# Performance work log

Measured on AMD Instinct MI355X. Metric: run time of the kernel, lower is better.

The kernel has to match this reference:

```python
import jax, jax.numpy as jnp
import numpy as np

NUM_HEADS = 8


def setup_inputs() -> dict:
    key = jax.random.key(0)
    ks = jax.random.split(key, 7)
    b, t, prompt_dim, emb_dim = 2, 4096, 256, 512
    hidden = emb_dim  # head_dim=None -> hidden_dim = emb_dim
    def xavier(k, fan_in, fan_out):
        limit = np.sqrt(6.0 / (fan_in + fan_out)).astype(np.float32)
        return jax.random.uniform(k, (fan_in, fan_out), jnp.float32, -limit, limit)
    return {
        "prompt": jax.random.normal(ks[0], (b, t, prompt_dim), jnp.float32),
        "Wp": xavier(ks[1], prompt_dim, emb_dim),
        "bp": jnp.zeros((emb_dim,), jnp.float32),
        "Wqkv": xavier(ks[2], emb_dim, 3 * hidden),
        "bqkv": jnp.zeros((3 * hidden,), jnp.float32),
        "Wo": xavier(ks[3], hidden, prompt_dim),
        "bo": jnp.zeros((prompt_dim,), jnp.float32),
    }


def reference(prompt, Wp, bp, Wqkv, bqkv, Wo, bo):
    # prompt_proj
    x = prompt @ Wp + bp                      # [b, t, emb_dim]
    b, t, c = x.shape
    qkv = x @ Wqkv + bqkv                     # [b, t, 3*hidden]
    q, k, v = jnp.split(qkv, 3, axis=2)
    def to_heads(z):
        return z.reshape(b, t, NUM_HEADS, -1).transpose(0, 2, 1, 3)  # [b, h, t, d]
    q, k, v = to_heads(q), to_heads(k), to_heads(v)
    d = k.shape[-1]
    scores = jnp.einsum("bhid,bhjd->bhij", q, k) / jnp.sqrt(jnp.float32(d))
    attn = jax.nn.softmax(scores, axis=-1)    # dropout = identity (eval)
    out = jnp.einsum("bhij,bhjd->bhid", attn, v)
    out = out.transpose(0, 2, 1, 3).reshape(b, t, -1)  # [b, t, hidden]
    return out @ Wo + bo                      # [b, t, prompt_dim]
```

## Files before the change

### kernel.cpp

```cpp
#include <hip/hip_runtime.h>
#include <math.h>
#include <stdint.h>


typedef unsigned short u16;
typedef __attribute__((ext_vector_type(8))) __bf16 bf16x8;
typedef __attribute__((ext_vector_type(4))) __bf16 bf16x4;
typedef __attribute__((ext_vector_type(4))) float f32x4;

#define AS1 __attribute__((address_space(1)))
#define AS3 __attribute__((address_space(3)))

__device__ __forceinline__ void async16(const void* g, void* l) {
  __builtin_amdgcn_global_load_lds((const AS1 void*)g, (AS3 void*)l, 16, 0, 0);
}

__device__ __forceinline__ u16 f2bf(float f) {
  union { float f; unsigned u; } c; c.f = f;
  return (u16)((c.u + 0x7fffu + ((c.u >> 16) & 1u)) >> 16);
}

__global__ void prep_kernel(const float* __restrict__ prompt, u16* __restrict__ pbf,
                            const float* __restrict__ Wp, u16* __restrict__ wpB,
                            const float* __restrict__ Wqkv, u16* __restrict__ wqkvT,
                            const float* __restrict__ Wo, u16* __restrict__ woT,
                            const float* __restrict__ bp, const float* __restrict__ bqkv,
                            float* __restrict__ bfused) {
  __shared__ u16 T[64][72];
  const int bid = blockIdx.x, tid = threadIdx.x;
  if (bid < 2688) {
    int i = bid * 256 + tid;
    if (i < 524288) {
      float4 v = ((const float4*)prompt)[i];
      ushort4 o;
      o.x = f2bf(v.x); o.y = f2bf(v.y); o.z = f2bf(v.z); o.w = f2bf(v.w);
      ((ushort4*)pbf)[i] = o;
    } else if (i < 557056) {
      int j = i - 524288;
      float4 v = ((const float4*)Wp)[j];
      ushort4 o;
      o.x = f2bf(v.x); o.y = f2bf(v.y); o.z = f2bf(v.z); o.w = f2bf(v.w);
      ((ushort4*)wpB)[j] = o;
    } else {
      int j = i - 557056; int n = j >> 9, k = j & 511;
      woT[j] = f2bf(Wo[k * 256 + n]);
    }
  } else if (bid < 2712) {
    __shared__ float red[256];
    const int nloc = tid & 63, slice = tid >> 6;
    const int n = (bid - 2688) * 64 + nloc;
    float s = 0.f;
#pragma unroll 8
    for (int e = slice * 128; e < slice * 128 + 128; e++) s += bp[e] * Wqkv[e * 1536 + n];
    red[tid] = s;
    __syncthreads();
    if (slice == 0)
      bfused[n] = red[nloc] + red[64 + nloc] + red[128 + nloc] + red[192 + nloc] + bqkv[n];
  } else {
    const int b = bid - 2712;
    const int k0 = (b & 7) * 64, n0 = (b >> 3) * 64;
    const int kl = tid >> 2, c4 = (tid & 3) * 16;
#pragma unroll
    for (int u = 0; u < 4; u++) {
      float4 v = *(const float4*)&Wqkv[(k0 + kl) * 1536 + n0 + c4 + 4 * u];
      T[kl][c4 + 4 * u + 0] = f2bf(v.x);
      T[kl][c4 + 4 * u + 1] = f2bf(v.y);
      T[kl][c4 + 4 * u + 2] = f2bf(v.z);
      T[kl][c4 + 4 * u + 3] = f2bf(v.w);
    }
    __syncthreads();
    const int nl = tid >> 2, kc = (tid & 3) * 16;
    u16 tmp[16];
#pragma unroll
    for (int e = 0; e < 16; e++) tmp[e] = T[kc + e][nl];
    *(uint4*)&wqkvT[(n0 + nl) * 512 + k0 + kc] = *(const uint4*)&tmp[0];
    *(uint4*)&wqkvT[(n0 + nl) * 512 + k0 + kc + 8] = *(const uint4*)&tmp[8];
  }
}

template <int TM, int TN, int MODE>
__global__ __launch_bounds__(256) void gemm_bt(
    const u16* __restrict__ A, const u16* __restrict__ Bt, const float* __restrict__ bias,
    float* __restrict__ outf, u16* __restrict__ outb,
    u16* __restrict__ qO, u16* __restrict__ kO, u16* __restrict__ vO,
    int M, int N, int K) {
  constexpr int MI = TM / 32, NJ = TN / 32;
  constexpr int NDMA = TM / 64 + TN / 64;
  __shared__ __align__(16) u16 As[2][TM * 32];
  __shared__ __align__(16) u16 Bs[2][TN * 32];
  const int tid = threadIdx.x;
  const int lane = tid & 63, w = tid >> 6;
  const int wr = w >> 1, wc = w & 1;
  const int lr = lane >> 4, lc = lane & 15;
  const long tileM = (long)blockIdx.y * TM;
  const long tileN = (long)blockIdx.x * TN;

  f32x4 acc[MI][NJ];
#pragma unroll
  for (int a = 0; a < MI; a++)
#pragma unroll
    for (int b = 0; b < NJ; b++) acc[a][b] = (f32x4){0.f, 0.f, 0.f, 0.f};

  const int r0 = lane >> 2;
  const int blk = lane & 3;

  auto stage = [&](int buf, int k0) {
#pragma unroll
    for (int i = 0; i < TM / 64; i++) {
      int r = w * (TM / 4) + i * 16 + r0;
      int g = (blk ^ ((r >> 1) & 3)) << 3;
      async16(A + (tileM + r) * (long)K + k0 + g, (void*)&As[buf][(w * (TM / 4) + i * 16) * 32]);
    }
#pragma unroll
    for (int i = 0; i < TN / 64; i++) {
      int r = w * (TN / 4) + i * 16 + r0;
      int g = (blk ^ ((r >> 1) & 3)) << 3;
      async16(Bt + (tileN + r) * (long)K + k0 + g, (void*)&Bs[buf][(w * (TN / 4) + i * 16) * 32]);
    }
  };

  stage(0, 0);
  for (int k0 = 0; k0 < K; k0 += 32) {
    const int cur = (k0 >> 5) & 1;
    stage(cur ^ 1, (k0 + 32 < K) ? k0 + 32 : 0);
    if constexpr (NDMA == 4) asm volatile("s_waitcnt vmcnt(4)" ::: "memory");
    else if constexpr (NDMA == 3) asm volatile("s_waitcnt vmcnt(3)" ::: "memory");
    else asm volatile("s_waitcnt vmcnt(2)" ::: "memory");
    asm volatile("s_barrier" ::: "memory");

    bf16x8 af[MI], bfv[NJ];
#pragma unroll
    for (int mi = 0; mi < MI; mi++) {
      int r = wr * (TM / 2) + mi * 16 + lc;
      af[mi] = *(const bf16x8*)&As[cur][r * 32 + ((lr ^ ((r >> 1) & 3)) << 3)];
    }
#pragma unroll
    for (int nj = 0; nj < NJ; nj++) {
      int r = wc * (TN / 2) + nj * 16 + lc;
      bfv[nj] = *(const bf16x8*)&Bs[cur][r * 32 + ((lr ^ ((r >> 1) & 3)) << 3)];
    }
#pragma unroll
    for (int mi = 0; mi < MI; mi++)
#pragma unroll
      for (int nj = 0; nj < NJ; nj++)
        acc[mi][nj] = __builtin_amdgcn_mfma_f32_16x16x32_bf16(af[mi], bfv[nj], acc[mi][nj], 0, 0, 0);
    asm volatile("s_barrier" ::: "memory");
  }

#pragma unroll
  for (int mi = 0; mi < MI; mi++)
#pragma unroll
    for (int nj = 0; nj < NJ; nj++) {
      long col = tileN + wc * (TN / 2) + nj * 16 + lc;
      long row0 = tileM + wr * (TM / 2) + mi * 16 + lr * 4;
      if constexpr (MODE == 1) {
        float bcol = bias[col];
        int sec = (int)(col >> 9);
        int c2 = (int)(col & 511);
        int h = c2 >> 6, d = c2 & 63;
        long pl = (row0 >> 12) * 8 + h;
        long t0 = row0 & 4095;
        if (sec == 2) {
          ushort4 pk;
          pk.x = f2bf(acc[mi][nj][0] + bcol);
          pk.y = f2bf(acc[mi][nj][1] + bcol);
          pk.z = f2bf(acc[mi][nj][2] + bcol);
          pk.w = f2bf(acc[mi][nj][3] + bcol);
          *(ushort4*)&vO[(pl * 64 + d) * 4096 + t0] = pk;
        } else {
          u16* dst = sec ? kO : qO;
          const float sc = sec ? 1.f : 0.18033688f;
#pragma unroll
          for (int r = 0; r < 4; r++)
            dst[((pl * 4096 + t0 + r) << 6) + d] = f2bf((acc[mi][nj][r] + bcol) * sc);
        }
      } else if constexpr (MODE == 2) {
        float bcol = bias[col];
#pragma unroll
        for (int r = 0; r < 4; r++)
          outf[(row0 + r) * (long)N + col] = acc[mi][nj][r] + bcol;
      } else {
#pragma unroll
        for (int r = 0; r < 4; r++)
          outb[(row0 + r) * (long)N + col] = f2bf(acc[mi][nj][r]);
      }
    }
}

__global__ __launch_bounds__(256) void flash_attn(
    const u16* __restrict__ Q, const u16* __restrict__ Kg,
    const u16* __restrict__ VTg, u16* __restrict__ Og) {
  __shared__ __align__(16) u16 KV[2][16384];
  __shared__ __align__(16) u16 Ps[4 * 2048];

  const int tid = threadIdx.x, lane = tid & 63, w = tid >> 6;
  const int lr = lane >> 4, lc = lane & 15;
  const int plane = blockIdx.y;
  const long pbase = (long)plane << 18;
  const int qr0 = blockIdx.x * 128 + w * 32;

  bf16x8 bq[2][2];
#pragma unroll
  for (int qi = 0; qi < 2; qi++)
#pragma unroll
    for (int kk = 0; kk < 2; kk++)
      bq[qi][kk] = *(const bf16x8*)&Q[pbase + (long)(qr0 + qi * 16 + lc) * 64 + kk * 32 + lr * 8];

  bf16x8 ones;
#pragma unroll
  for (int u = 0; u < 8; u++) ones[u] = (__bf16)1.0f;

  f32x4 o[2][4], o1[2];
#pragma unroll
  for (int mi = 0; mi < 2; mi++) {
    o1[mi] = (f32x4){0.f, 0.f, 0.f, 0.f};
#pragma unroll
    for (int nj = 0; nj < 4; nj++) o[mi][nj] = (f32x4){0.f, 0.f, 0.f, 0.f};
  }

  const int krow = lane >> 3, kblk = lane & 7;
  const int vrow = lane >> 4, vblk = lane & 15;

  auto stage = [&](int buf, int j) {
    const u16* kS = Kg + pbase + (long)j * 8192;
    const u16* vS = VTg + pbase + j * 128;
#pragma unroll
    for (int i = 0; i < 4; i++) {
      int row = w * 32 + i * 8 + krow;
      async16(kS + (long)row * 64 + ((kblk ^ (row & 7)) << 3), (void*)&KV[buf][w * 2048 + i * 512]);
    }
#pragma unroll
    for (int i = 0; i < 4; i++) {
      int d = w * 16 + i * 4 + vrow;
      async16(vS + (long)d * 4096 + ((vblk ^ (d & 7)) << 3), (void*)&KV[buf][8192 + w * 2048 + i * 512]);
    }
  };

  stage(0, 0);
  for (int j = 0; j < 32; j++) {
    const int cur = j & 1;
    stage(cur ^ 1, (j + 1) & 31);
    asm volatile("s_waitcnt vmcnt(8)" ::: "memory");
    asm volatile("s_barrier" ::: "memory");

    const u16* Ks = &KV[cur][0];
    const u16* Vt = &KV[cur][8192];

    f32x4 s[8][2];
#pragma unroll
    for (int ki = 0; ki < 8; ki++)
#pragma unroll
      for (int qi = 0; qi < 2; qi++) s[ki][qi] = (f32x4){0.f, 0.f, 0.f, 0.f};
#pragma unroll
    for (int ki = 0; ki < 8; ki++) {
      bf16x8 ak[2];
#pragma unroll
      for (int kk = 0; kk < 2; kk++)
        ak[kk] = *(const bf16x8*)&Ks[(ki * 16 + lc) * 64 + (((kk * 4 + lr) ^ (lc & 7)) << 3)];
#pragma unroll
      for (int qi = 0; qi < 2; qi++)
#pragma unroll
        for (int kk = 0; kk < 2; kk++)
          s[ki][qi] = __builtin_amdgcn_mfma_f32_16x16x32_bf16(ak[kk], bq[qi][kk], s[ki][qi], 0, 0, 0);
    }

#pragma unroll
    for (int hh = 0; hh < 2; hh++) {
#pragma unroll
      for (int qi = 0; qi < 2; qi++) {
        const int pb = w * 2048 + (qi * 16 + lc) * 64 + 4 * (lr & 1);
#pragma unroll
        for (int kp = 0; kp < 4; kp++) {
          const int ki = 4 * hh + kp;
          bf16x4 pk;
          pk[0] = (__bf16)__builtin_amdgcn_exp2f(s[ki][qi][0]);
          pk[1] = (__bf16)__builtin_amdgcn_exp2f(s[ki][qi][1]);
          pk[2] = (__bf16)__builtin_amdgcn_exp2f(s[ki][qi][2]);
          pk[3] = (__bf16)__builtin_amdgcn_exp2f(s[ki][qi][3]);
          *(bf16x4*)&Ps[pb + (((2 * kp + (lr >> 1)) ^ (lc & 7)) << 3)] = pk;
        }
      }
#pragma unroll
      for (int kk = 0; kk < 2; kk++) {
        bf16x8 ap[2];
#pragma unroll
        for (int mi = 0; mi < 2; mi++)
          ap[mi] = *(const bf16x8*)&Ps[w * 2048 + (mi * 16 + lc) * 64 + (((4 * kk + lr) ^ (lc & 7)) << 3)];
#pragma unroll
        for (int nj = 0; nj < 4; nj++) {
          bf16x8 bv = *(const bf16x8*)&Vt[(nj * 16 + lc) * 128 + ((((hh * 2 + kk) * 4 + lr) ^ (lc & 7)) << 3)];
#pragma unroll
          for (int mi = 0; mi < 2; mi++)
            o[mi][nj] = __builtin_amdgcn_mfma_f32_16x16x32_bf16(ap[mi], bv, o[mi][nj], 0, 0, 0);
        }
#pragma unroll
        for (int mi = 0; mi < 2; mi++)
          o1[mi] = __builtin_amdgcn_mfma_f32_16x16x32_bf16(ap[mi], ones, o1[mi], 0, 0, 0);
      }
    }
    asm volatile("s_barrier" ::: "memory");
  }

  const int bb = plane >> 3, h = plane & 7;
#pragma unroll
  for (int mi = 0; mi < 2; mi++)
#pragma unroll
    for (int r = 0; r < 4; r++) {
      float inv = 1.f / o1[mi][r];
      long t = qr0 + mi * 16 + 4 * lr + r;
#pragma unroll
      for (int nj = 0; nj < 4; nj++)
        Og[(((long)(bb * 4096 + t) * 8 + h) << 6) + nj * 16 + lc] = f2bf(o[mi][nj][r] * inv);
    }
}

extern "C" void kernel_launch(void* const* d_in, const int* in_sizes, int n_in,
                              void* d_out, int out_size, void* d_ws, size_t ws_size,
                              hipStream_t stream) {
  const float* prompt = (const float*)d_in[0];
  const float* Wp = (const float*)d_in[1];
  const float* bp = (const float*)d_in[2];
  const float* Wqkv = (const float*)d_in[3];
  const float* bqkv = (const float*)d_in[4];
  const float* Wo = (const float*)d_in[5];
  const float* bo = (const float*)d_in[6];
  float* out = (float*)d_out;

  char* ws = (char*)d_ws;
  const size_t MiB = 1024 * 1024;
  u16* attnO  = (u16*)(ws + 0);
  u16* qb     = (u16*)(ws + 8 * MiB);
  u16* kb     = (u16*)(ws + 16 * MiB);
  u16* vb     = (u16*)(ws + 24 * MiB);
  u16* pbf    = (u16*)(ws + 32 * MiB);
  u16* wpB    = (u16*)(ws + 36 * MiB);
  u16* wqkvT  = (u16*)(ws + 36 * MiB + 256 * 1024);
  u16* woT    = (u16*)(ws + 36 * MiB + 1792 * 1024);
  u16* wfT    = (u16*)(ws + 36 * MiB + 2048 * 1024);
  float* bfused = (float*)(ws + 36 * MiB + 2816 * 1024);

  prep_kernel<<<dim3(2904), dim3(256), 0, stream>>>(
      prompt, pbf, Wp, wpB, Wqkv, wqkvT, Wo, woT, bp, bqkv, bfused);

  gemm_bt<64, 64, 3><<<dim3(4, 24), dim3(256), 0, stream>>>(
      wqkvT, wpB, nullptr, nullptr, wfT, nullptr, nullptr, nullptr, 1536, 256, 512);
  gemm_bt<128, 128, 1><<<dim3(12, 64), dim3(256), 0, stream>>>(
      pbf, wfT, bfused, nullptr, nullptr, qb, kb, vb, 8192, 1536, 256);
  flash_attn<<<dim3(32, 16), dim3(256), 0, stream>>>(qb, kb, vb, attnO);
  gemm_bt<64, 64, 2><<<dim3(4, 128), dim3(256), 0, stream>>>(
      attnO, woT, bo, out, nullptr, nullptr, nullptr, nullptr, 8192, 256, 512);
}
```

Measured before the change: 203.8 us.

## Fuse output projection into flash attention and weight-fusion GEMM into prep

Each flash-attention block now multiplies its normalized per-head output tile by the matching 64-row slice of Wo, loaded into shared memory. It accumulates the result into the fp32 output with atomicAdd, after the prep kernel pre-fills the output with the bias bo. The Wqkv·Wp weight fusion also moves into the prep kernel as an in-kernel MFMA GEMM, so the separate weight-fusion GEMM launch and the bf16 attention-output round trip are gone. The cost is 8-way atomic contention per output element and a non-deterministic summation order across heads.

```diff
diff --git a/kernel.cpp b/kernel.cpp
--- a/kernel.cpp
+++ b/kernel.cpp
@@ -21,34 +21,69 @@
 }
 
 __global__ void prep_kernel(const float* __restrict__ prompt, u16* __restrict__ pbf,
-                            const float* __restrict__ Wp, u16* __restrict__ wpB,
-                            const float* __restrict__ Wqkv, u16* __restrict__ wqkvT,
+                            const float* __restrict__ Wp, const float* __restrict__ Wqkv,
                             const float* __restrict__ Wo, u16* __restrict__ woT,
                             const float* __restrict__ bp, const float* __restrict__ bqkv,
-                            float* __restrict__ bfused) {
-  __shared__ u16 T[64][72];
+                            float* __restrict__ bfused, u16* __restrict__ wfT,
+                            const float* __restrict__ bo, float* __restrict__ outp) {
+  __shared__ u16 Asf[64 * 40];
+  __shared__ u16 Bsf[64 * 32];
+  __shared__ float red[256];
   const int bid = blockIdx.x, tid = threadIdx.x;
-  if (bid < 2688) {
-    int i = bid * 256 + tid;
-    if (i < 524288) {
-      float4 v = ((const float4*)prompt)[i];
-      ushort4 o;
-      o.x = f2bf(v.x); o.y = f2bf(v.y); o.z = f2bf(v.z); o.w = f2bf(v.w);
-      ((ushort4*)pbf)[i] = o;
-    } else if (i < 557056) {
-      int j = i - 524288;
-      float4 v = ((const float4*)Wp)[j];
-      ushort4 o;
-      o.x = f2bf(v.x); o.y = f2bf(v.y); o.z = f2bf(v.z); o.w = f2bf(v.w);
-      ((ushort4*)wpB)[j] = o;
-    } else {
-      int j = i - 557056; int n = j >> 9, k = j & 511;
-      woT[j] = f2bf(Wo[k * 256 + n]);
-    }
-  } else if (bid < 2712) {
-    __shared__ float red[256];
+  if (bid < 96) {
+    const int k0 = (bid & 3) * 64, n0 = (bid >> 2) * 64;
+    const int lane = tid & 63, w = tid >> 6;
+    const int wr = w >> 1, wc = w & 1;
+    const int lr = lane >> 4, lc = lane & 15;
+    f32x4 acc[2][2];
+#pragma unroll
+    for (int a = 0; a < 2; a++)
+#pragma unroll
+      for (int b = 0; b < 2; b++) acc[a][b] = (f32x4){0.f, 0.f, 0.f, 0.f};
+    for (int e0 = 0; e0 < 512; e0 += 32) {
+      {
+        const int er = tid >> 3, ng = (tid & 7) * 8;
+        float4 v1 = *(const float4*)&Wqkv[(e0 + er) * 1536 + n0 + ng];
+        float4 v2 = *(const float4*)&Wqkv[(e0 + er) * 1536 + n0 + ng + 4];
+        Asf[(ng + 0) * 40 + er] = f2bf(v1.x); Asf[(ng + 1) * 40 + er] = f2bf(v1.y);
+        Asf[(ng + 2) * 40 + er] = f2bf(v1.z); Asf[(ng + 3) * 40 + er] = f2bf(v1.w);
+        Asf[(ng + 4) * 40 + er] = f2bf(v2.x); Asf[(ng + 5) * 40 + er] = f2bf(v2.y);
+        Asf[(ng + 6) * 40 + er] = f2bf(v2.z); Asf[(ng + 7) * 40 + er] = f2bf(v2.w);
+      }
+      {
+        const int kr = tid >> 2, ec = (tid & 3) * 8;
+        float4 w1 = *(const float4*)&Wp[(k0 + kr) * 512 + e0 + ec];
+        float4 w2 = *(const float4*)&Wp[(k0 + kr) * 512 + e0 + ec + 4];
+        u16 tmp[8] = {f2bf(w1.x), f2bf(w1.y), f2bf(w1.z), f2bf(w1.w),
+                      f2bf(w2.x), f2bf(w2.y), f2bf(w2.z), f2bf(w2.w)};
+        *(uint4*)&Bsf[kr * 32 + ec] = *(const uint4*)&tmp[0];
+      }
+      __syncthreads();
+      bf16x8 af[2], bf2[2];
+#pragma unroll
+      for (int mi = 0; mi < 2; mi++)
+        af[mi] = *(const bf16x8*)&Asf[(wr * 32 + mi * 16 + lc) * 40 + lr * 8];
+#pragma unroll
+      for (int nj = 0; nj < 2; nj++)
+        bf2[nj] = *(const bf16x8*)&Bsf[(wc * 32 + nj * 16 + lc) * 32 + lr * 8];
+#pragma unroll
+      for (int mi = 0; mi < 2; mi++)
+#pragma unroll
+        for (int nj = 0; nj < 2; nj++)
+          acc[mi][nj] = __builtin_amdgcn_mfma_f32_16x16x32_bf16(af[mi], bf2[nj], acc[mi][nj], 0, 0, 0);
+      __syncthreads();
+    }
+#pragma unroll
+    for (int mi = 0; mi < 2; mi++)
+#pragma unroll
+      for (int nj = 0; nj < 2; nj++)
+#pragma unroll
+        for (int r = 0; r < 4; r++)
+          wfT[(n0 + wr * 32 + mi * 16 + 4 * lr + r) * 256 + k0 + wc * 32 + nj * 16 + lc] =
+              f2bf(acc[mi][nj][r]);
+  } else if (bid < 120) {
     const int nloc = tid & 63, slice = tid >> 6;
-    const int n = (bid - 2688) * 64 + nloc;
+    const int n = (bid - 96) * 64 + nloc;
     float s = 0.f;
 #pragma unroll 8
     for (int e = slice * 128; e < slice * 128 + 128; e++) s += bp[e] * Wqkv[e * 1536 + n];
@@ -56,36 +91,26 @@
     __syncthreads();
     if (slice == 0)
       bfused[n] = red[nloc] + red[64 + nloc] + red[128 + nloc] + red[192 + nloc] + bqkv[n];
+  } else if (bid < 632) {
+    int j = (bid - 120) * 256 + tid;
+    int n = j >> 9, k = j & 511;
+    woT[j] = f2bf(Wo[k * 256 + n]);
+  } else if (bid < 2680) {
+    int i = (bid - 632) * 256 + tid;
+    float4 v = ((const float4*)prompt)[i];
+    ushort4 o;
+    o.x = f2bf(v.x); o.y = f2bf(v.y); o.z = f2bf(v.z); o.w = f2bf(v.w);
+    ((ushort4*)pbf)[i] = o;
   } else {
-    const int b = bid - 2712;
-    const int k0 = (b & 7) * 64, n0 = (b >> 3) * 64;
-    const int kl = tid >> 2, c4 = (tid & 3) * 16;
-#pragma unroll
-    for (int u = 0; u < 4; u++) {
-      float4 v = *(const float4*)&Wqkv[(k0 + kl) * 1536 + n0 + c4 + 4 * u];
-      T[kl][c4 + 4 * u + 0] = f2bf(v.x);
-      T[kl][c4 + 4 * u + 1] = f2bf(v.y);
-      T[kl][c4 + 4 * u + 2] = f2bf(v.z);
-      T[kl][c4 + 4 * u + 3] = f2bf(v.w);
-    }
-    __syncthreads();
-    const int nl = tid >> 2, kc = (tid & 3) * 16;
-    u16 tmp[16];
-#pragma unroll
-    for (int e = 0; e < 16; e++) tmp[e] = T[kc + e][nl];
-    *(uint4*)&wqkvT[(n0 + nl) * 512 + k0 + kc] = *(const uint4*)&tmp[0];
-    *(uint4*)&wqkvT[(n0 + nl) * 512 + k0 + kc + 8] = *(const uint4*)&tmp[8];
-  }
-}
-
-template <int TM, int TN, int MODE>
-__global__ __launch_bounds__(256) void gemm_bt(
+    int i = (bid - 2680) * 256 + tid;
+    ((float4*)outp)[i] = ((const float4*)bo)[i & 63];
+  }
+}
+
+__global__ __launch_bounds__(256) void gemm_qkv(
     const u16* __restrict__ A, const u16* __restrict__ Bt, const float* __restrict__ bias,
-    float* __restrict__ outf, u16* __restrict__ outb,
-    u16* __restrict__ qO, u16* __restrict__ kO, u16* __restrict__ vO,
-    int M, int N, int K) {
-  constexpr int MI = TM / 32, NJ = TN / 32;
-  constexpr int NDMA = TM / 64 + TN / 64;
+    u16* __restrict__ qO, u16* __restrict__ kO, u16* __restrict__ vO, int K) {
+  constexpr int TM = 128, TN = 128, MI = 4, NJ = 4;
   __shared__ __align__(16) u16 As[2][TM * 32];
   __shared__ __align__(16) u16 Bs[2][TN * 32];
   const int tid = threadIdx.x;
@@ -106,16 +131,11 @@
 
   auto stage = [&](int buf, int k0) {
 #pragma unroll
-    for (int i = 0; i < TM / 64; i++) {
-      int r = w * (TM / 4) + i * 16 + r0;
+    for (int i = 0; i < 2; i++) {
+      int r = w * 32 + i * 16 + r0;
       int g = (blk ^ ((r >> 1) & 3)) << 3;
-      async16(A + (tileM + r) * (long)K + k0 + g, (void*)&As[buf][(w * (TM / 4) + i * 16) * 32]);
-    }
-#pragma unroll
-    for (int i = 0; i < TN / 64; i++) {
-      int r = w * (TN / 4) + i * 16 + r0;
-      int g = (blk ^ ((r >> 1) & 3)) << 3;
-      async16(Bt + (tileN + r) * (long)K + k0 + g, (void*)&Bs[buf][(w * (TN / 4) + i * 16) * 32]);
+      async16(A + (tileM + r) * (long)K + k0 + g, (void*)&As[buf][(w * 32 + i * 16) * 32]);
+      async16(Bt + (tileN + r) * (long)K + k0 + g, (void*)&Bs[buf][(w * 32 + i * 16) * 32]);
     }
   };
 
@@ -123,20 +143,18 @@
   for (int k0 = 0; k0 < K; k0 += 32) {
     const int cur = (k0 >> 5) & 1;
     stage(cur ^ 1, (k0 + 32 < K) ? k0 + 32 : 0);
-    if constexpr (NDMA == 4) asm volatile("s_waitcnt vmcnt(4)" ::: "memory");
-    else if constexpr (NDMA == 3) asm volatile("s_waitcnt vmcnt(3)" ::: "memory");
-    else asm volatile("s_waitcnt vmcnt(2)" ::: "memory");
+    asm volatile("s_waitcnt vmcnt(4)" ::: "memory");
     asm volatile("s_barrier" ::: "memory");
 
     bf16x8 af[MI], bfv[NJ];
 #pragma unroll
     for (int mi = 0; mi < MI; mi++) {
-      int r = wr * (TM / 2) + mi * 16 + lc;
+      int r = wr * 64 + mi * 16 + lc;
       af[mi] = *(const bf16x8*)&As[cur][r * 32 + ((lr ^ ((r >> 1) & 3)) << 3)];
     }
 #pragma unroll
     for (int nj = 0; nj < NJ; nj++) {
-      int r = wc * (TN / 2) + nj * 16 + lc;
+      int r = wc * 64 + nj * 16 + lc;
       bfv[nj] = *(const bf16x8*)&Bs[cur][r * 32 + ((lr ^ ((r >> 1) & 3)) << 3)];
     }
 #pragma unroll
@@ -151,45 +169,35 @@
   for (int mi = 0; mi < MI; mi++)
 #pragma unroll
     for (int nj = 0; nj < NJ; nj++) {
-      long col = tileN + wc * (TN / 2) + nj * 16 + lc;
-      long row0 = tileM + wr * (TM / 2) + mi * 16 + lr * 4;
-      if constexpr (MODE == 1) {
-        float bcol = bias[col];
-        int sec = (int)(col >> 9);
-        int c2 = (int)(col & 511);
-        int h = c2 >> 6, d = c2 & 63;
-        long pl = (row0 >> 12) * 8 + h;
-        long t0 = row0 & 4095;
-        if (sec == 2) {
-          ushort4 pk;
-          pk.x = f2bf(acc[mi][nj][0] + bcol);
-          pk.y = f2bf(acc[mi][nj][1] + bcol);
-          pk.z = f2bf(acc[mi][nj][2] + bcol);
-          pk.w = f2bf(acc[mi][nj][3] + bcol);
-          *(ushort4*)&vO[(pl * 64 + d) * 4096 + t0] = pk;
-        } else {
-          u16* dst = sec ? kO : qO;
-          const float sc = sec ? 1.f : 0.18033688f;
-#pragma unroll
-          for (int r = 0; r < 4; r++)
-            dst[((pl * 4096 + t0 + r) << 6) + d] = f2bf((acc[mi][nj][r] + bcol) * sc);
-        }
-      } else if constexpr (MODE == 2) {
-        float bcol = bias[col];
+      long col = tileN + wc * 64 + nj * 16 + lc;
+      float bcol = bias[col];
+      long row0 = tileM + wr * 64 + mi * 16 + lr * 4;
+      int sec = (int)(col >> 9);
+      int c2 = (int)(col & 511);
+      int h = c2 >> 6, d = c2 & 63;
+      long pl = (row0 >> 12) * 8 + h;
+      long t0 = row0 & 4095;
+      if (sec == 2) {
+        ushort4 pk;
+        pk.x = f2bf(acc[mi][nj][0] + bcol);
+        pk.y = f2bf(acc[mi][nj][1] + bcol);
+        pk.z = f2bf(acc[mi][nj][2] + bcol);
+        pk.w = f2bf(acc[mi][nj][3] + bcol);
+        *(ushort4*)&vO[(pl * 64 + d) * 4096 + t0] = pk;
+      } else {
+        u16* dst = sec ? kO : qO;
+        const float sc = sec ? 1.f : 0.18033688f;
 #pragma unroll
         for (int r = 0; r < 4; r++)
-          outf[(row0 + r) * (long)N + col] = acc[mi][nj][r] + bcol;
-      } else {
-#pragma unroll
-        for (int r = 0; r < 4; r++)
-          outb[(row0 + r) * (long)N + col] = f2bf(acc[mi][nj][r]);
+          dst[((pl * 4096 + t0 + r) << 6) + d] = f2bf((acc[mi][nj][r] + bcol) * sc);
       }
     }
 }
 
 __global__ __launch_bounds__(256) void flash_attn(
     const u16* __restrict__ Q, const u16* __restrict__ Kg,
-    const u16* __restrict__ VTg, u16* __restrict__ Og) {
+    const u16* __restrict__ VTg, const u16* __restrict__ WoTg,
+    float* __restrict__ outp) {
   __shared__ __align__(16) u16 KV[2][16384];
   __shared__ __align__(16) u16 Ps[4 * 2048];
 
@@ -301,17 +309,59 @@
     asm volatile("s_barrier" ::: "memory");
   }
 
-  const int bb = plane >> 3, h = plane & 7;
+  asm volatile("s_waitcnt vmcnt(0)" ::: "memory");
+  asm volatile("s_barrier" ::: "memory");
+  {
+    const u16* wS = WoTg + (plane & 7) * 64;
+#pragma unroll
+    for (int i = 0; i < 8; i++) {
+      int rowb = i * 32 + w * 8;
+      int row = rowb + (lane >> 3);
+      int src = ((lane & 7) ^ (row & 7)) << 3;
+      async16(wS + (long)row * 512 + src, (void*)&KV[0][rowb * 64]);
+    }
+  }
 #pragma unroll
   for (int mi = 0; mi < 2; mi++)
 #pragma unroll
     for (int r = 0; r < 4; r++) {
       float inv = 1.f / o1[mi][r];
-      long t = qr0 + mi * 16 + 4 * lr + r;
-#pragma unroll
-      for (int nj = 0; nj < 4; nj++)
-        Og[(((long)(bb * 4096 + t) * 8 + h) << 6) + nj * 16 + lc] = f2bf(o[mi][nj][r] * inv);
-    }
+      int qloc = mi * 16 + 4 * lr + r;
+#pragma unroll
+      for (int nj = 0; nj < 4; nj++) {
+        int d = nj * 16 + lc;
+        Ps[w * 2048 + qloc * 64 + (((d >> 3) ^ (qloc & 7)) << 3) + (d & 7)] =
+            f2bf(o[mi][nj][r] * inv);
+      }
+    }
+  asm volatile("s_waitcnt vmcnt(0)" ::: "memory");
+  asm volatile("s_barrier" ::: "memory");
+
+  bf16x8 ap2[2][2];
+#pragma unroll
+  for (int mi = 0; mi < 2; mi++)
+#pragma unroll
+    for (int kk = 0; kk < 2; kk++)
+      ap2[mi][kk] = *(const bf16x8*)&Ps[w * 2048 + (mi * 16 + lc) * 64 + (((kk * 4 + lr) ^ (lc & 7)) << 3)];
+  const long tb = (long)(plane >> 3) * 4096 + qr0;
+#pragma unroll
+  for (int nb = 0; nb < 16; nb++) {
+    f32x4 a2[2];
+    a2[0] = (f32x4){0.f, 0.f, 0.f, 0.f};
+    a2[1] = (f32x4){0.f, 0.f, 0.f, 0.f};
+#pragma unroll
+    for (int kk = 0; kk < 2; kk++) {
+      bf16x8 bw = *(const bf16x8*)&KV[0][(nb * 16 + lc) * 64 + (((kk * 4 + lr) ^ (lc & 7)) << 3)];
+#pragma unroll
+      for (int mi = 0; mi < 2; mi++)
+        a2[mi] = __builtin_amdgcn_mfma_f32_16x16x32_bf16(ap2[mi][kk], bw, a2[mi], 0, 0, 0);
+    }
+#pragma unroll
+    for (int mi = 0; mi < 2; mi++)
+#pragma unroll
+      for (int r = 0; r < 4; r++)
+        atomicAdd(&outp[(tb + mi * 16 + 4 * lr + r) * 256 + nb * 16 + lc], a2[mi][r]);
+  }
 }
 
 extern "C" void kernel_launch(void* const* d_in, const int* in_sizes, int n_in,
@@ -328,25 +378,19 @@
 
   char* ws = (char*)d_ws;
   const size_t MiB = 1024 * 1024;
-  u16* attnO  = (u16*)(ws + 0);
-  u16* qb     = (u16*)(ws + 8 * MiB);
-  u16* kb     = (u16*)(ws + 16 * MiB);
-  u16* vb     = (u16*)(ws + 24 * MiB);
-  u16* pbf    = (u16*)(ws + 32 * MiB);
-  u16* wpB    = (u16*)(ws + 36 * MiB);
-  u16* wqkvT  = (u16*)(ws + 36 * MiB + 256 * 1024);
-  u16* woT    = (u16*)(ws + 36 * MiB + 1792 * 1024);
-  u16* wfT    = (u16*)(ws + 36 * MiB + 2048 * 1024);
-  float* bfused = (float*)(ws + 36 * MiB + 2816 * 1024);
-
-  prep_kernel<<<dim3(2904), dim3(256), 0, stream>>>(
-      prompt, pbf, Wp, wpB, Wqkv, wqkvT, Wo, woT, bp, bqkv, bfused);
-
-  gemm_bt<64, 64, 3><<<dim3(4, 24), dim3(256), 0, stream>>>(
-      wqkvT, wpB, nullptr, nullptr, wfT, nullptr, nullptr, nullptr, 1536, 256, 512);
-  gemm_bt<128, 128, 1><<<dim3(12, 64), dim3(256), 0, stream>>>(
-      pbf, wfT, bfused, nullptr, nullptr, qb, kb, vb, 8192, 1536, 256);
-  flash_attn<<<dim3(32, 16), dim3(256), 0, stream>>>(qb, kb, vb, attnO);
-  gemm_bt<64, 64, 2><<<dim3(4, 128), dim3(256), 0, stream>>>(
-      attnO, woT, bo, out, nullptr, nullptr, nullptr, nullptr, 8192, 256, 512);
-}
+  u16* qb     = (u16*)(ws + 0);
+  u16* kb     = (u16*)(ws + 8 * MiB);
+  u16* vb     = (u16*)(ws + 16 * MiB);
+  u16* pbf    = (u16*)(ws + 24 * MiB);
+  u16* woT    = (u16*)(ws + 28 * MiB);
+  u16* wfT    = (u16*)(ws + 28 * MiB + 256 * 1024);
+  float* bfused = (float*)(ws + 28 * MiB + 1024 * 1024);
+
+  prep_kernel<<<dim3(4728), dim3(256), 0, stream>>>(
+      prompt, pbf, Wp, Wqkv, Wo, woT, bp, bqkv, bfused, wfT, bo, out);
+
+  gemm_qkv<<<dim3(12, 64), dim3(256), 0, stream>>>(
+      pbf, wfT, bfused, qb, kb, vb, 256);
+
+  flash_attn<<<dim3(32, 16), dim3(256), 0, stream>>>(qb, kb, vb, woT, out);
+}
```

Result: slower. 229.8 us (+12.8%).
